# Performance work log

Measured on AMD Instinct MI355X. Metric: run time of the kernel, lower is better.

## Reference

```python
import jax, jax.numpy as jnp
import numpy as np

VOCAB = 100000
EMBED = 128
MAX_LEN = 200
NUM_GENRES = 20  # ml-20m genre count; index NUM_GENRES is the 'unknown' pad genre
MAX_G = 8        # max genres per movie (padded ragged width)


def setup_inputs() -> dict:
    key = jax.random.key(0)
    ks = jax.random.split(key, 6)
    sequence = jax.random.randint(ks[0], (256, 200), 0, VOCAB)
    token_table = jax.random.normal(ks[1], (VOCAB, EMBED), dtype=jnp.float32)
    genre_table = jax.random.normal(ks[2], (NUM_GENRES + 1, EMBED), dtype=jnp.float32)
    pos_table = jax.random.normal(ks[3], (MAX_LEN, EMBED), dtype=jnp.float32)
    # padded ragged genre mapping per token: ids in [0, NUM_GENRES], counts in [1, MAX_G]
    token_genre_ids = jax.random.randint(ks[4], (VOCAB, MAX_G), 0, NUM_GENRES + 1)
    genre_counts = jax.random.randint(ks[5], (VOCAB,), 1, MAX_G + 1)
    return {
        "sequence": sequence,
        "token_table": token_table,
        "genre_table": genre_table,
        "pos_table": pos_table,
        "token_genre_ids": token_genre_ids,
        "genre_counts": genre_counts,
    }


def reference(sequence, token_table, genre_table, pos_table, token_genre_ids, genre_counts):
    B, L = sequence.shape
    # token embedding: [B, L, D]
    tok = token_table[sequence]
    # ragged genre mean: gather padded genre ids per token, mask, mean
    gids = token_genre_ids[sequence]                       # [B, L, G]
    counts = genre_counts[sequence]                        # [B, L]
    mask = (jnp.arange(MAX_G) < counts[..., None]).astype(token_table.dtype)  # [B, L, G]
    ge = genre_table[gids]                                 # [B, L, G, D]
    genre_mean = jnp.einsum("blgd,blg->bld", ge, mask) / counts[..., None].astype(token_table.dtype)
    # positional embedding: [L, D] broadcast over batch
    pos = pos_table[:L]
    # dropout is identity in eval mode
    return tok + genre_mean + pos[None, :, :]
```

## Files before the change

kernel.cpp:

```cpp
#include <hip/hip_runtime.h>

#define B_SZ   256
#define L_SZ   200
#define EMBED  128
#define MAX_G  8
#define NTOK   (B_SZ * L_SZ)
#define F4_PER_ROW (EMBED / 4)

__global__ __launch_bounds__(256) void bert_embed_kernel(
    const int*    __restrict__ seq,
    const float4* __restrict__ tok_tab,
    const float4* __restrict__ gen_tab,
    const float4* __restrict__ pos_tab,
    const int*    __restrict__ tgid,
    const int*    __restrict__ gcnt,
    float4*       __restrict__ out)
{
    const int tid   = threadIdx.x;
    const int group = tid >> 5;
    const int lane  = tid & 31;

    const int token_idx = blockIdx.x * 8 + group;
    if (token_idx >= NTOK) return;

    const int l = token_idx % L_SZ;
    const int t = seq[token_idx];

    float4 acc = tok_tab[(long)t * F4_PER_ROW + lane];

    const float4 p = pos_tab[l * F4_PER_ROW + lane];
    acc.x += p.x; acc.y += p.y; acc.z += p.z; acc.w += p.w;

    const int cnt = gcnt[t];
    const int* g = tgid + (long)t * MAX_G;
    float4 gs; gs.x = 0.f; gs.y = 0.f; gs.z = 0.f; gs.w = 0.f;
    #pragma unroll 1
    for (int i = 0; i < cnt; ++i) {
        const int gid = g[i];
        const float4 ge = gen_tab[gid * F4_PER_ROW + lane];
        gs.x += ge.x; gs.y += ge.y; gs.z += ge.z; gs.w += ge.w;
    }
    const float inv = 1.0f / (float)cnt;
    acc.x += gs.x * inv; acc.y += gs.y * inv;
    acc.z += gs.z * inv; acc.w += gs.w * inv;

    out[(long)token_idx * F4_PER_ROW + lane] = acc;
}

extern "C" void kernel_launch(void* const* d_in, const int* in_sizes, int n_in,
                              void* d_out, int out_size, void* d_ws, size_t ws_size,
                              hipStream_t stream) {
    const int*    seq     = (const int*)   d_in[0];
    const float4* tok_tab = (const float4*)d_in[1];
    const float4* gen_tab = (const float4*)d_in[2];
    const float4* pos_tab = (const float4*)d_in[3];
    const int*    tgid    = (const int*)   d_in[4];
    const int*    gcnt    = (const int*)   d_in[5];
    float4*       out     = (float4*)      d_out;

    const int blocks = (NTOK + 7) / 8;
    bert_embed_kernel<<<blocks, 256, 0, stream>>>(seq, tok_tab, gen_tab,
                                                  pos_tab, tgid, gcnt, out);
}
```

Measured before the change: 113.1 us.

## Process two tokens per warp-group with branchless unrolled genre gathers and nontemporal stores

Each 32-lane group now handles two tokens, one from each half of the sequence batch, and issues all of their loads up front. Genre ids are read as two int4 vectors and all eight genre rows are gathered unconditionally, with masked weights in an unrolled FMA loop replacing the data-dependent serial loop. Output is written with nontemporal stores so it does not pollute the cache. The aim is more memory-level parallelism and less dependent-load latency, at the cost of more registers and some redundant genre-row loads, which are cheap because the genre table is small.

```diff
diff --git a/kernel.cpp b/kernel.cpp
--- a/kernel.cpp
+++ b/kernel.cpp
@@ -5,7 +5,10 @@
 #define EMBED  128
 #define MAX_G  8
 #define NTOK   (B_SZ * L_SZ)
+#define HALF   (NTOK / 2)
 #define F4_PER_ROW (EMBED / 4)
+
+typedef float nativef4 __attribute__((ext_vector_type(4)));
 
 __global__ __launch_bounds__(256) void bert_embed_kernel(
     const int*    __restrict__ seq,
@@ -20,31 +23,64 @@
     const int group = tid >> 5;
     const int lane  = tid & 31;
 
-    const int token_idx = blockIdx.x * 8 + group;
-    if (token_idx >= NTOK) return;
+    const int idx0 = blockIdx.x * 8 + group;
+    const int idx1 = idx0 + HALF;
+    if (idx0 >= HALF) return;
 
-    const int l = token_idx % L_SZ;
-    const int t = seq[token_idx];
+    const int t0 = seq[idx0];
+    const int t1 = seq[idx1];
+    const float4 p0 = pos_tab[(idx0 % L_SZ) * F4_PER_ROW + lane];
+    const float4 p1 = pos_tab[(idx1 % L_SZ) * F4_PER_ROW + lane];
 
-    float4 acc = tok_tab[(long)t * F4_PER_ROW + lane];
+    const float4 tokv0 = tok_tab[(long)t0 * F4_PER_ROW + lane];
+    const float4 tokv1 = tok_tab[(long)t1 * F4_PER_ROW + lane];
+    const int cnt0 = gcnt[t0];
+    const int cnt1 = gcnt[t1];
+    const int4* g40 = (const int4*)(tgid + (long)t0 * MAX_G);
+    const int4* g41 = (const int4*)(tgid + (long)t1 * MAX_G);
+    const int4 ga0 = g40[0], gb0 = g40[1];
+    const int4 ga1 = g41[0], gb1 = g41[1];
+    const int gid0[MAX_G] = { ga0.x, ga0.y, ga0.z, ga0.w, gb0.x, gb0.y, gb0.z, gb0.w };
+    const int gid1[MAX_G] = { ga1.x, ga1.y, ga1.z, ga1.w, gb1.x, gb1.y, gb1.z, gb1.w };
 
-    const float4 p = pos_tab[l * F4_PER_ROW + lane];
-    acc.x += p.x; acc.y += p.y; acc.z += p.z; acc.w += p.w;
+    float4 r0[MAX_G], r1[MAX_G];
+    #pragma unroll
+    for (int i = 0; i < MAX_G; ++i) r0[i] = gen_tab[gid0[i] * F4_PER_ROW + lane];
+    #pragma unroll
+    for (int i = 0; i < MAX_G; ++i) r1[i] = gen_tab[gid1[i] * F4_PER_ROW + lane];
 
-    const int cnt = gcnt[t];
-    const int* g = tgid + (long)t * MAX_G;
-    float4 gs; gs.x = 0.f; gs.y = 0.f; gs.z = 0.f; gs.w = 0.f;
-    #pragma unroll 1
-    for (int i = 0; i < cnt; ++i) {
-        const int gid = g[i];
-        const float4 ge = gen_tab[gid * F4_PER_ROW + lane];
-        gs.x += ge.x; gs.y += ge.y; gs.z += ge.z; gs.w += ge.w;
+    {
+        const float inv = 1.0f / (float)cnt0;
+        nativef4 acc;
+        acc.x = tokv0.x + p0.x; acc.y = tokv0.y + p0.y;
+        acc.z = tokv0.z + p0.z; acc.w = tokv0.w + p0.w;
+        #pragma unroll
+        for (int i = 0; i < MAX_G; ++i) {
+            const float w = (i < cnt0) ? inv : 0.0f;
+            acc.x = fmaf(w, r0[i].x, acc.x);
+            acc.y = fmaf(w, r0[i].y, acc.y);
+            acc.z = fmaf(w, r0[i].z, acc.z);
+            acc.w = fmaf(w, r0[i].w, acc.w);
+        }
+        __builtin_nontemporal_store(acc,
+            (nativef4*)&out[(long)idx0 * F4_PER_ROW + lane]);
     }
-    const float inv = 1.0f / (float)cnt;
-    acc.x += gs.x * inv; acc.y += gs.y * inv;
-    acc.z += gs.z * inv; acc.w += gs.w * inv;
-
-    out[(long)token_idx * F4_PER_ROW + lane] = acc;
+    {
+        const float inv = 1.0f / (float)cnt1;
+        nativef4 acc;
+        acc.x = tokv1.x + p1.x; acc.y = tokv1.y + p1.y;
+        acc.z = tokv1.z + p1.z; acc.w = tokv1.w + p1.w;
+        #pragma unroll
+        for (int i = 0; i < MAX_G; ++i) {
+            const float w = (i < cnt1) ? inv : 0.0f;
+            acc.x = fmaf(w, r1[i].x, acc.x);
+            acc.y = fmaf(w, r1[i].y, acc.y);
+            acc.z = fmaf(w, r1[i].z, acc.z);
+            acc.w = fmaf(w, r1[i].w, acc.w);
+        }
+        __builtin_nontemporal_store(acc,
+            (nativef4*)&out[(long)idx1 * F4_PER_ROW + lane]);
+    }
 }
 
 extern "C" void kernel_launch(void* const* d_in, const int* in_sizes, int n_in,
@@ -58,7 +94,7 @@
     const int*    gcnt    = (const int*)   d_in[5];
     float4*       out     = (float4*)      d_out;
 
-    const int blocks = (NTOK + 7) / 8;
+    const int blocks = HALF / 8;
     bert_embed_kernel<<<blocks, 256, 0, stream>>>(seq, tok_tab, gen_tab,
                                                   pos_tab, tgid, gcnt, out);
 }
```

New measurement: 112.1 us. Within noise of the previous version (-0.9%).
